# Kernel tuning notes

Hardware: AMD Instinct MI355X
Metric: run time of the kernel (lower is better)

The kernel has to match this reference:

```python
import jax, jax.numpy as jnp
import numpy as np

N_NODES = 50000
N_EDGES = 800000
EMB = 100
LAYERS = 3
EPS = 1e-12  # torch F.normalize default eps


def setup_inputs() -> dict:
    key = jax.random.key(0)
    k1, k2, k3, k4 = jax.random.split(key, 4)
    adj_row = jax.random.randint(k1, (N_EDGES,), 0, N_NODES, dtype=jnp.int32)
    adj_col = jax.random.randint(k2, (N_EDGES,), 0, N_NODES, dtype=jnp.int32)
    adj_val = jax.random.uniform(k3, (N_EDGES,), dtype=jnp.float32)
    embedding = jax.random.normal(k4, (N_NODES, EMB), dtype=jnp.float32)
    a = jnp.ones((LAYERS + 1, 1, 1), dtype=jnp.float32)  # init.ones_
    return {"adj_row": adj_row, "adj_col": adj_col, "adj_val": adj_val,
            "embedding": embedding, "a": a}


def reference(adj_row, adj_col, adj_val, embedding, a):
    def spmm(x):
        # sparse.mm(A, x): gather source rows, scale by edge value, scatter-add to dest rows
        return jax.ops.segment_sum(adj_val[:, None] * x[adj_col], adj_row,
                                   num_segments=N_NODES)

    outs = [embedding]
    x = embedding
    for _ in range(LAYERS):
        x = spmm(x)
        outs.append(x)
    final = jnp.stack(outs, axis=0)  # [L+1, N, d]
    # F.normalize(..., dim=-1, p=2): x / max(||x||_2, eps)
    norm = jnp.sqrt(jnp.sum(final * final, axis=-1, keepdims=True))
    final = final / jnp.maximum(norm, EPS)
    return jnp.sum(a * final, axis=0)  # [N, d]
```

## Files before the change

kernel.cpp:

```cpp
#include <hip/hip_runtime.h>
#include <hip/hip_bf16.h>

#define N_NODES 50000
#define N_EDGES 800000
#define EMB 100
#define HALF_EMB 50
#define ROW_U4 16
#define ROW_B2 64
#define NORM_EPS 1e-12f
#define BROWS 128
#define NB ((N_NODES + BROWS - 1) / BROWS)
#define CAP 4096
#define EPB 16384
#define SCAT_BLOCKS ((N_EDGES + EPB - 1) / EPB)
#define CONV_BLOCKS 3125

#define SEL_LO 0x01000504u
#define SEL_HI 0x03020706u

__global__ __launch_bounds__(1024) void scatter_conv(
        const int* __restrict__ adj_row, const int* __restrict__ adj_col,
        const float* __restrict__ adj_val, int* __restrict__ bucket_cnt,
        int2* __restrict__ slab,
        const float* __restrict__ emb, float* __restrict__ norm0,
        __hip_bfloat162* __restrict__ xb) {
    const int t = threadIdx.x;
    if (blockIdx.x >= SCAT_BLOCKS) {
        int wave = (blockIdx.x - SCAT_BLOCKS) * 16 + (t >> 6);
        int lane = t & 63;
        if (wave >= N_NODES) return;
        float2 v = make_float2(0.0f, 0.0f);
        if (lane < HALF_EMB) v = ((const float2*)emb)[(size_t)wave * HALF_EMB + lane];
        float s = v.x * v.x + v.y * v.y;
        #pragma unroll
        for (int off = 32; off > 0; off >>= 1) s += __shfl_xor(s, off);
        if (lane == 0) norm0[wave] = sqrtf(s);
        __hip_bfloat162 b;
        b.x = __float2bfloat16(v.x);
        b.y = __float2bfloat16(v.y);
        xb[(size_t)wave * ROW_B2 + lane] = b;
        return;
    }
    __shared__ int hist[NB];
    __shared__ int cur[NB];
    const int base_e = blockIdx.x * EPB;
    for (int i = t; i < NB; i += 1024) hist[i] = 0;
    __syncthreads();
    int rows[EPB / 1024];
    #pragma unroll
    for (int j = 0; j < EPB / 1024; ++j) {
        int e = base_e + j * 1024 + t;
        int r = (e < N_EDGES) ? adj_row[e] : -1;
        rows[j] = r;
        if (r >= 0) atomicAdd(&hist[r >> 7], 1);
    }
    __syncthreads();
    for (int i = t; i < NB; i += 1024) {
        int c = hist[i];
        cur[i] = (c > 0) ? atomicAdd(&bucket_cnt[i], c) : 0;
    }
    __syncthreads();
    #pragma unroll
    for (int j = 0; j < EPB / 1024; ++j) {
        int e = base_e + j * 1024 + t;
        int r = rows[j];
        if (r >= 0) {
            int b = r >> 7;
            int p = atomicAdd(&cur[b], 1);
            unsigned rc = ((unsigned)r << 16) | (unsigned)adj_col[e];
            slab[(size_t)b * CAP + p] = make_int2((int)rc, __float_as_int(adj_val[e]));
        }
    }
}

__global__ __launch_bounds__(1024) void csr_build(
        const int* __restrict__ bucket_cnt, const int2* __restrict__ slab,
        unsigned* __restrict__ csr4, int* __restrict__ row_ptr) {
    __shared__ int hist[BROWS];
    __shared__ int wsum[16];
    __shared__ int wtot[2];
    __shared__ int base_sh;
    const int b = blockIdx.x, t = threadIdx.x;
    const int lane = t & 63, wid = t >> 6;
    int pv = (t < b) ? bucket_cnt[t] : 0;
    #pragma unroll
    for (int off = 32; off > 0; off >>= 1) pv += __shfl_xor(pv, off);
    if (lane == 0) wsum[wid] = pv;
    if (t < BROWS) hist[t] = 0;
    const int cnt = bucket_cnt[b];
    __syncthreads();
    if (t == 0) {
        int s_ = 0;
        #pragma unroll
        for (int i = 0; i < 16; ++i) s_ += wsum[i];
        base_sh = s_;
    }
    for (int i = t; i < cnt; i += 1024)
        atomicAdd(&hist[(int)(((unsigned)slab[(size_t)b * CAP + i].x) >> 16) & (BROWS - 1)], 1);
    __syncthreads();
    const int base = base_sh;
    int v = (t < BROWS) ? hist[t] : 0;
    int sc = v;
    #pragma unroll
    for (int off = 1; off < 64; off <<= 1) {
        int n = __shfl_up(sc, off);
        if (lane >= off) sc += n;
    }
    if (t < BROWS && lane == 63) wtot[wid] = sc;
    __syncthreads();
    if (wid == 1 && t < BROWS) sc += wtot[0];
    int ex = sc - v;
    if (t < BROWS) {
        hist[t] = ex;
        int gr = b * BROWS + t;
        if (gr < N_NODES) row_ptr[gr] = base + ex;
    }
    if (b == 0 && t == 0) row_ptr[N_NODES] = N_EDGES;
    __syncthreads();
    for (int i = t; i < cnt; i += 1024) {
        int2 e = slab[(size_t)b * CAP + i];
        int l = (int)(((unsigned)e.x) >> 16) & (BROWS - 1);
        int p = atomicAdd(&hist[l], 1);
        unsigned col = (unsigned)e.x & 0xFFFFu;
        __hip_bfloat16 hv = __float2bfloat16(__int_as_float(e.y));
        unsigned vb = (unsigned)*reinterpret_cast<unsigned short*>(&hv);
        csr4[base + p] = (col << 16) | vb;
    }
}

__device__ inline float dot2b(unsigned a, unsigned b, float c) {
    float d;
    asm("v_dot2_f32_bf16 %0, %1, %2, %3" : "=v"(d) : "v"(a), "v"(b), "v"(c));
    return d;
}

__device__ inline void dot8pair(unsigned ra, unsigned rb, uint4 ua, uint4 ub,
                                float4& accL, float4& accH) {
    unsigned vp = __builtin_amdgcn_perm(ra, rb, SEL_LO);
    accL.x = dot2b(vp, __builtin_amdgcn_perm(ua.x, ub.x, SEL_LO), accL.x);
    accL.y = dot2b(vp, __builtin_amdgcn_perm(ua.x, ub.x, SEL_HI), accL.y);
    accL.z = dot2b(vp, __builtin_amdgcn_perm(ua.y, ub.y, SEL_LO), accL.z);
    accL.w = dot2b(vp, __builtin_amdgcn_perm(ua.y, ub.y, SEL_HI), accL.w);
    accH.x = dot2b(vp, __builtin_amdgcn_perm(ua.z, ub.z, SEL_LO), accH.x);
    accH.y = dot2b(vp, __builtin_amdgcn_perm(ua.z, ub.z, SEL_HI), accH.y);
    accH.z = dot2b(vp, __builtin_amdgcn_perm(ua.w, ub.w, SEL_LO), accH.z);
    accH.w = dot2b(vp, __builtin_amdgcn_perm(ua.w, ub.w, SEL_HI), accH.w);
}

__device__ inline void up8(uint4 u, float4& lo, float4& hi) {
    lo.x = __uint_as_float(u.x << 16);
    lo.y = __uint_as_float(u.x & 0xFFFF0000u);
    lo.z = __uint_as_float(u.y << 16);
    lo.w = __uint_as_float(u.y & 0xFFFF0000u);
    hi.x = __uint_as_float(u.z << 16);
    hi.y = __uint_as_float(u.z & 0xFFFF0000u);
    hi.z = __uint_as_float(u.w << 16);
    hi.w = __uint_as_float(u.w & 0xFFFF0000u);
}

__device__ inline unsigned pack2(float a, float b) {
    __hip_bfloat16 x = __float2bfloat16(a), y = __float2bfloat16(b);
    return (unsigned)*(unsigned short*)&x | ((unsigned)*(unsigned short*)&y << 16);
}

__global__ void spmm_fused(const int* __restrict__ row_ptr,
                           const unsigned* __restrict__ csr4,
                           const uint4* __restrict__ xb,
                           uint4* __restrict__ yb,
                           float* __restrict__ norm_out,
                           const float* __restrict__ a,
                           const uint4* __restrict__ ep0,
                           const uint4* __restrict__ ep1,
                           const float* __restrict__ norms,
                           float* __restrict__ out,
                           int final_layer) {
    int wave = blockIdx.x * (blockDim.x >> 6) + (threadIdx.x >> 6);
    int lane = threadIdx.x & 63;
    if (wave >= N_NODES) return;
    int start = row_ptr[wave];
    int end   = row_ptr[wave + 1];
    int deg   = end - start;
    unsigned myrec = (lane < deg) ? csr4[start + lane] : 0u;
    int g = lane >> 4, c = lane & 15;
    float4 accL = make_float4(0.0f, 0.0f, 0.0f, 0.0f);
    float4 accH = make_float4(0.0f, 0.0f, 0.0f, 0.0f);
    int dn  = (deg < 64) ? deg : 64;
    int dn4 = (dn + 3) & ~3;
    int d = 0;
    for (; d + 16 <= dn4; d += 16) {
        unsigned ra = __shfl(myrec, d + g);
        unsigned rb = __shfl(myrec, d + 4 + g);
        unsigned rc = __shfl(myrec, d + 8 + g);
        unsigned rd = __shfl(myrec, d + 12 + g);
        uint4 ua = xb[(size_t)(ra >> 16) * ROW_U4 + c];
        uint4 ub = xb[(size_t)(rb >> 16) * ROW_U4 + c];
        uint4 uc = xb[(size_t)(rc >> 16) * ROW_U4 + c];
        uint4 ud = xb[(size_t)(rd >> 16) * ROW_U4 + c];
        dot8pair(ra, rb, ua, ub, accL, accH);
        dot8pair(rc, rd, uc, ud, accL, accH);
    }
    for (; d + 8 <= dn4; d += 8) {
        unsigned ra = __shfl(myrec, d + g);
        unsigned rb = __shfl(myrec, d + 4 + g);
        uint4 ua = xb[(size_t)(ra >> 16) * ROW_U4 + c];
        uint4 ub = xb[(size_t)(rb >> 16) * ROW_U4 + c];
        dot8pair(ra, rb, ua, ub, accL, accH);
    }
    for (; d < dn4; d += 4) {
        unsigned r = __shfl(myrec, d + g);
        uint4 u = xb[(size_t)(r >> 16) * ROW_U4 + c];
        float v = __uint_as_float(r << 16);
        float4 l, h;
        up8(u, l, h);
        accL.x += v * l.x; accL.y += v * l.y; accL.z += v * l.z; accL.w += v * l.w;
        accH.x += v * h.x; accH.y += v * h.y; accH.z += v * h.z; accH.w += v * h.w;
    }
    for (int e = start + 64; e < end; e += 4) {
        unsigned r = (e + g < end) ? csr4[e + g] : 0u;
        uint4 u = xb[(size_t)(r >> 16) * ROW_U4 + c];
        float v = __uint_as_float(r << 16);
        float4 l, h;
        up8(u, l, h);
        accL.x += v * l.x; accL.y += v * l.y; accL.z += v * l.z; accL.w += v * l.w;
        accH.x += v * h.x; accH.y += v * h.y; accH.z += v * h.z; accH.w += v * h.w;
    }
    accL.x += __shfl_xor(accL.x, 16); accL.x += __shfl_xor(accL.x, 32);
    accL.y += __shfl_xor(accL.y, 16); accL.y += __shfl_xor(accL.y, 32);
    accL.z += __shfl_xor(accL.z, 16); accL.z += __shfl_xor(accL.z, 32);
    accL.w += __shfl_xor(accL.w, 16); accL.w += __shfl_xor(accL.w, 32);
    accH.x += __shfl_xor(accH.x, 16); accH.x += __shfl_xor(accH.x, 32);
    accH.y += __shfl_xor(accH.y, 16); accH.y += __shfl_xor(accH.y, 32);
    accH.z += __shfl_xor(accH.z, 16); accH.z += __shfl_xor(accH.z, 32);
    accH.w += __shfl_xor(accH.w, 16); accH.w += __shfl_xor(accH.w, 32);
    float s = accL.x * accL.x + accL.y * accL.y + accL.z * accL.z + accL.w * accL.w
            + accH.x * accH.x + accH.y * accH.y + accH.z * accH.z + accH.w * accH.w;
    s += __shfl_xor(s, 1); s += __shfl_xor(s, 2);
    s += __shfl_xor(s, 4); s += __shfl_xor(s, 8);
    if (!final_layer) {
        if (g == 0) {
            uint4 o;
            o.x = pack2(accL.x, accL.y);
            o.y = pack2(accL.z, accL.w);
            o.z = pack2(accH.x, accH.y);
            o.w = pack2(accH.z, accH.w);
            yb[(size_t)wave * ROW_U4 + c] = o;
        }
        if (lane == 0) norm_out[wave] = sqrtf(s);
    } else {
        float s0 = a[0] / fmaxf(norms[wave], NORM_EPS);
        float s1 = a[1] / fmaxf(norms[N_NODES + wave], NORM_EPS);
        float s2 = a[2] / fmaxf(norms[2 * N_NODES + wave], NORM_EPS);
        float s3 = a[3] / fmaxf(sqrtf(s), NORM_EPS);
        if (g == 0 && c < 13) {
            size_t idx = (size_t)wave * ROW_U4 + c;
            float4 f0l, f0h, f1l, f1h, f2l, f2h;
            up8(ep0[idx], f0l, f0h);
            up8(ep1[idx], f1l, f1h);
            up8(xb[idx],  f2l, f2h);
            float4 o0, o1;
            o0.x = s0 * f0l.x + s1 * f1l.x + s2 * f2l.x + s3 * accL.x;
            o0.y = s0 * f0l.y + s1 * f1l.y + s2 * f2l.y + s3 * accL.y;
            o0.z = s0 * f0l.z + s1 * f1l.z + s2 * f2l.z + s3 * accL.z;
            o0.w = s0 * f0l.w + s1 * f1l.w + s2 * f2l.w + s3 * accL.w;
            o1.x = s0 * f0h.x + s1 * f1h.x + s2 * f2h.x + s3 * accH.x;
            o1.y = s0 * f0h.y + s1 * f1h.y + s2 * f2h.y + s3 * accH.y;
            o1.z = s0 * f0h.z + s1 * f1h.z + s2 * f2h.z + s3 * accH.z;
            o1.w = s0 * f0h.w + s1 * f1h.w + s2 * f2h.w + s3 * accH.w;
            float4* out4 = (float4*)out;
            size_t fb = (size_t)wave * 25;
            if (c < 12) {
                out4[fb + 2 * c]     = o0;
                out4[fb + 2 * c + 1] = o1;
            } else {
                out4[fb + 24] = o0;
            }
        }
    }
}

extern "C" void kernel_launch(void* const* d_in, const int* in_sizes, int n_in,
                              void* d_out, int out_size, void* d_ws, size_t ws_size,
                              hipStream_t stream) {
    const int*   adj_row   = (const int*)d_in[0];
    const int*   adj_col   = (const int*)d_in[1];
    const float* adj_val   = (const float*)d_in[2];
    const float* embedding = (const float*)d_in[3];
    const float* a         = (const float*)d_in[4];
    float* out = (float*)d_out;

    int2* slab     = (int2*)d_ws;
    unsigned* csr4 = (unsigned*)(slab + (size_t)NB * CAP);
    uint4* xbE = (uint4*)(csr4 + N_EDGES);
    uint4* xb1 = xbE + (size_t)N_NODES * ROW_U4;
    float* norms = (float*)(xb1 + (size_t)N_NODES * ROW_U4);
    int* row_ptr    = (int*)(norms + 3 * N_NODES);
    int* bucket_cnt = row_ptr + (N_NODES + 1);
    uint4* xb2 = (uint4*)slab;

    const int node_blocks = (N_NODES + 3) / 4;

    hipMemsetAsync(bucket_cnt, 0, sizeof(int) * NB, stream);
    scatter_conv<<<SCAT_BLOCKS + CONV_BLOCKS, 1024, 0, stream>>>(
        adj_row, adj_col, adj_val, bucket_cnt, slab,
        embedding, norms, (__hip_bfloat162*)xbE);
    csr_build<<<NB, 1024, 0, stream>>>(bucket_cnt, slab, csr4, row_ptr);

    spmm_fused<<<node_blocks, 256, 0, stream>>>(row_ptr, csr4, xbE,
                                                xb1, norms + N_NODES, a,
                                                nullptr, nullptr, nullptr,
                                                nullptr, 0);
    spmm_fused<<<node_blocks, 256, 0, stream>>>(row_ptr, csr4, xb1,
                                                xb2, norms + 2 * N_NODES, a,
                                                nullptr, nullptr, nullptr,
                                                nullptr, 0);
    spmm_fused<<<node_blocks, 256, 0, stream>>>(row_ptr, csr4, xb2,
                                                nullptr, nullptr, a,
                                                xbE, xb1, norms,
                                                out, 1);
}
```

Measured before the change: 216.4 us.

## Stage CSR bucket in LDS, shrink scatter tile, replace dot2 with FMA path

Cuts edges per scatter block from 16384 to 4096, so more blocks share the bucketing work. csr_build now copies each bucket's slab into shared memory once and reuses it for both the histogram and placement passes. Its wave-shuffle reductions and scans become shared-memory tree loops with many __syncthreads. The spmm loop drops the packed bf16 v_dot2 path for plain per-edge FMAs on unpacked bf16 values, and turns the 8- and 4-edge tail loops into single if-steps. This trades extra ALU work and barriers for simpler code and fewer global reads of the slab.

```diff
diff --git a/kernel.cpp b/kernel.cpp
--- a/kernel.cpp
+++ b/kernel.cpp
@@ -11,12 +11,9 @@
 #define BROWS 128
 #define NB ((N_NODES + BROWS - 1) / BROWS)
 #define CAP 4096
-#define EPB 16384
+#define EPB 4096
 #define SCAT_BLOCKS ((N_EDGES + EPB - 1) / EPB)
 #define CONV_BLOCKS 3125
-
-#define SEL_LO 0x01000504u
-#define SEL_HI 0x03020706u
 
 __global__ __launch_bounds__(1024) void scatter_conv(
         const int* __restrict__ adj_row, const int* __restrict__ adj_col,
@@ -76,49 +73,45 @@
 __global__ __launch_bounds__(1024) void csr_build(
         const int* __restrict__ bucket_cnt, const int2* __restrict__ slab,
         unsigned* __restrict__ csr4, int* __restrict__ row_ptr) {
+    __shared__ int2 eds[CAP];
     __shared__ int hist[BROWS];
-    __shared__ int wsum[16];
-    __shared__ int wtot[2];
-    __shared__ int base_sh;
+    __shared__ int incl[BROWS];
+    __shared__ int red[1024];
     const int b = blockIdx.x, t = threadIdx.x;
-    const int lane = t & 63, wid = t >> 6;
-    int pv = (t < b) ? bucket_cnt[t] : 0;
-    #pragma unroll
-    for (int off = 32; off > 0; off >>= 1) pv += __shfl_xor(pv, off);
-    if (lane == 0) wsum[wid] = pv;
+    red[t] = (t < b) ? bucket_cnt[t] : 0;
+    __syncthreads();
+    #pragma unroll
+    for (int off = 512; off > 0; off >>= 1) {
+        if (t < off) red[t] += red[t + off];
+        __syncthreads();
+    }
+    const int base = red[0];
+    const int cnt = bucket_cnt[b];
+    for (int i = t; i < cnt; i += 1024) eds[i] = slab[(size_t)b * CAP + i];
     if (t < BROWS) hist[t] = 0;
-    const int cnt = bucket_cnt[b];
-    __syncthreads();
-    if (t == 0) {
-        int s_ = 0;
-        #pragma unroll
-        for (int i = 0; i < 16; ++i) s_ += wsum[i];
-        base_sh = s_;
-    }
+    __syncthreads();
     for (int i = t; i < cnt; i += 1024)
-        atomicAdd(&hist[(int)(((unsigned)slab[(size_t)b * CAP + i].x) >> 16) & (BROWS - 1)], 1);
-    __syncthreads();
-    const int base = base_sh;
+        atomicAdd(&hist[(int)(((unsigned)eds[i].x) >> 16) & (BROWS - 1)], 1);
+    __syncthreads();
     int v = (t < BROWS) ? hist[t] : 0;
-    int sc = v;
-    #pragma unroll
-    for (int off = 1; off < 64; off <<= 1) {
-        int n = __shfl_up(sc, off);
-        if (lane >= off) sc += n;
-    }
-    if (t < BROWS && lane == 63) wtot[wid] = sc;
-    __syncthreads();
-    if (wid == 1 && t < BROWS) sc += wtot[0];
-    int ex = sc - v;
-    if (t < BROWS) {
-        hist[t] = ex;
-        int gr = b * BROWS + t;
-        if (gr < N_NODES) row_ptr[gr] = base + ex;
-    }
+    if (t < BROWS) incl[t] = v;
+    __syncthreads();
+    #pragma unroll
+    for (int off = 1; off < BROWS; off <<= 1) {
+        int n = (t >= off && t < BROWS) ? incl[t - off] : 0;
+        __syncthreads();
+        if (t < BROWS) incl[t] += n;
+        __syncthreads();
+    }
+    int ex = (t < BROWS) ? (incl[t] - v) : 0;
+    __syncthreads();
+    if (t < BROWS) hist[t] = ex;
+    int gr = b * BROWS + t;
+    if (t < BROWS && gr < N_NODES) row_ptr[gr] = base + ex;
     if (b == 0 && t == 0) row_ptr[N_NODES] = N_EDGES;
     __syncthreads();
     for (int i = t; i < cnt; i += 1024) {
-        int2 e = slab[(size_t)b * CAP + i];
+        int2 e = eds[i];
         int l = (int)(((unsigned)e.x) >> 16) & (BROWS - 1);
         int p = atomicAdd(&hist[l], 1);
         unsigned col = (unsigned)e.x & 0xFFFFu;
@@ -126,25 +119,6 @@
         unsigned vb = (unsigned)*reinterpret_cast<unsigned short*>(&hv);
         csr4[base + p] = (col << 16) | vb;
     }
-}
-
-__device__ inline float dot2b(unsigned a, unsigned b, float c) {
-    float d;
-    asm("v_dot2_f32_bf16 %0, %1, %2, %3" : "=v"(d) : "v"(a), "v"(b), "v"(c));
-    return d;
-}
-
-__device__ inline void dot8pair(unsigned ra, unsigned rb, uint4 ua, uint4 ub,
-                                float4& accL, float4& accH) {
-    unsigned vp = __builtin_amdgcn_perm(ra, rb, SEL_LO);
-    accL.x = dot2b(vp, __builtin_amdgcn_perm(ua.x, ub.x, SEL_LO), accL.x);
-    accL.y = dot2b(vp, __builtin_amdgcn_perm(ua.x, ub.x, SEL_HI), accL.y);
-    accL.z = dot2b(vp, __builtin_amdgcn_perm(ua.y, ub.y, SEL_LO), accL.z);
-    accL.w = dot2b(vp, __builtin_amdgcn_perm(ua.y, ub.y, SEL_HI), accL.w);
-    accH.x = dot2b(vp, __builtin_amdgcn_perm(ua.z, ub.z, SEL_LO), accH.x);
-    accH.y = dot2b(vp, __builtin_amdgcn_perm(ua.z, ub.z, SEL_HI), accH.y);
-    accH.z = dot2b(vp, __builtin_amdgcn_perm(ua.w, ub.w, SEL_LO), accH.z);
-    accH.w = dot2b(vp, __builtin_amdgcn_perm(ua.w, ub.w, SEL_HI), accH.w);
 }
 
 __device__ inline void up8(uint4 u, float4& lo, float4& hi) {
@@ -161,6 +135,14 @@
 __device__ inline unsigned pack2(float a, float b) {
     __hip_bfloat16 x = __float2bfloat16(a), y = __float2bfloat16(b);
     return (unsigned)*(unsigned short*)&x | ((unsigned)*(unsigned short*)&y << 16);
+}
+
+__device__ inline void fma_edge(unsigned r, uint4 u, float4& accL, float4& accH) {
+    float v = __uint_as_float(r << 16);
+    float4 l, h;
+    up8(u, l, h);
+    accL.x += v * l.x; accL.y += v * l.y; accL.z += v * l.z; accL.w += v * l.w;
+    accH.x += v * h.x; accH.y += v * h.y; accH.z += v * h.z; accH.w += v * h.w;
 }
 
 __global__ void spmm_fused(const int* __restrict__ row_ptr,
@@ -196,33 +178,29 @@
         uint4 ub = xb[(size_t)(rb >> 16) * ROW_U4 + c];
         uint4 uc = xb[(size_t)(rc >> 16) * ROW_U4 + c];
         uint4 ud = xb[(size_t)(rd >> 16) * ROW_U4 + c];
-        dot8pair(ra, rb, ua, ub, accL, accH);
-        dot8pair(rc, rd, uc, ud, accL, accH);
-    }
-    for (; d + 8 <= dn4; d += 8) {
+        fma_edge(ra, ua, accL, accH);
+        fma_edge(rb, ub, accL, accH);
+        fma_edge(rc, uc, accL, accH);
+        fma_edge(rd, ud, accL, accH);
+    }
+    if (d + 8 <= dn4) {
         unsigned ra = __shfl(myrec, d + g);
         unsigned rb = __shfl(myrec, d + 4 + g);
         uint4 ua = xb[(size_t)(ra >> 16) * ROW_U4 + c];
         uint4 ub = xb[(size_t)(rb >> 16) * ROW_U4 + c];
-        dot8pair(ra, rb, ua, ub, accL, accH);
-    }
-    for (; d < dn4; d += 4) {
+        fma_edge(ra, ua, accL, accH);
+        fma_edge(rb, ub, accL, accH);
+        d += 8;
+    }
+    if (d < dn4) {
         unsigned r = __shfl(myrec, d + g);
         uint4 u = xb[(size_t)(r >> 16) * ROW_U4 + c];
-        float v = __uint_as_float(r << 16);
-        float4 l, h;
-        up8(u, l, h);
-        accL.x += v * l.x; accL.y += v * l.y; accL.z += v * l.z; accL.w += v * l.w;
-        accH.x += v * h.x; accH.y += v * h.y; accH.z += v * h.z; accH.w += v * h.w;
+        fma_edge(r, u, accL, accH);
     }
     for (int e = start + 64; e < end; e += 4) {
         unsigned r = (e + g < end) ? csr4[e + g] : 0u;
         uint4 u = xb[(size_t)(r >> 16) * ROW_U4 + c];
-        float v = __uint_as_float(r << 16);
-        float4 l, h;
-        up8(u, l, h);
-        accL.x += v * l.x; accL.y += v * l.y; accL.z += v * l.z; accL.w += v * l.w;
-        accH.x += v * h.x; accH.y += v * h.y; accH.z += v * h.z; accH.w += v * h.w;
+        fma_edge(r, u, accL, accH);
     }
     accL.x += __shfl_xor(accL.x, 16); accL.x += __shfl_xor(accL.x, 32);
     accL.y += __shfl_xor(accL.y, 16); accL.y += __shfl_xor(accL.y, 32);
```

After: 198.8 us. 1.09x faster.
